# Optimization experiments

Hardware: AMD Instinct MI355X
Metric: run time of the kernel (lower is better)

The kernel has to match this reference:

```python
import jax, jax.numpy as jnp
import numpy as np

B, S, D, H = 2, 2048, 1024, 16
HD = D // H  # 64
ROPE_BASE = 10000.0


def _rope_tables(seq_len, head_dim):
    pos = jnp.arange(seq_len, dtype=jnp.float32)
    inv_freq = 1.0 / (ROPE_BASE ** (jnp.arange(0, head_dim, 2, dtype=jnp.float32) / head_dim))
    ang = pos[:, None] * inv_freq[None, :]            # [S, HD/2]
    emb = jnp.concatenate([ang, ang], axis=-1)        # [S, HD]
    return jnp.cos(emb), jnp.sin(emb)


def setup_inputs() -> dict:
    key = jax.random.key(0)
    k0, k1, k2 = jax.random.split(key, 3)
    x = jax.random.normal(k0, (B, S, D), dtype=jnp.float32)
    Wq = jax.random.normal(k1, (D, D), dtype=jnp.float32) * 0.02
    Wv = jax.random.normal(k2, (D, D), dtype=jnp.float32) * 0.02
    cos, sin = _rope_tables(S, HD)
    return {"x": x, "Wq": Wq, "Wv": Wv, "cos": cos, "sin": sin}


def _rotate_half(u):
    h = u.shape[-1] // 2
    return jnp.concatenate([-u[..., h:], u[..., :h]], axis=-1)


def reference(x, Wq, Wv, cos, sin):
    b, s, d = x.shape
    h, hd = H, d // H
    # NOTE: source module has xk = self.query(x) (key uses query weights) -- preserved.
    xq = (x @ Wq.T).reshape(b, s, h, hd)
    xk = (x @ Wq.T).reshape(b, s, h, hd)
    xv = (x @ Wv.T).reshape(b, s, h, hd)
    c = cos[None, :, None, :]  # [1,S,1,HD]
    sn = sin[None, :, None, :]
    q = xq * c + _rotate_half(xq) * sn
    k = xk * c + _rotate_half(xk) * sn
    q = q.transpose(0, 2, 1, 3)   # [B,H,S,HD]
    k = k.transpose(0, 2, 1, 3)
    v = xv.transpose(0, 2, 1, 3)
    scale = 1.0 / jnp.sqrt(jnp.asarray(hd, dtype=q.dtype))
    scores = jnp.einsum('bhqd,bhkd->bhqk', q, k) * scale  # [B,H,S,S]
    causal = jnp.tril(jnp.ones((s, s), dtype=bool))
    scores = jnp.where(causal[None, None, :, :], scores, jnp.finfo(scores.dtype).min)
    probs = jax.nn.softmax(scores, axis=-1)
    out = jnp.einsum('bhqk,bhkd->bhqd', probs, v)
    return out.transpose(0, 2, 1, 3).reshape(b, s, d)
```

## Files before the change

kernel.cpp:

```cpp
#include <hip/hip_runtime.h>


typedef float f32x4 __attribute__((ext_vector_type(4)));
typedef short s16x8 __attribute__((ext_vector_type(8)));

__device__ inline unsigned short f2bf(float f) {
  union { float f; unsigned u; } v; v.f = f;
  unsigned r = v.u + 0x7FFFu + ((v.u >> 16) & 1u);
  return (unsigned short)(r >> 16);
}

__device__ inline void gload16(const unsigned short* g, unsigned short* l) {
  __builtin_amdgcn_global_load_lds(
      (const __attribute__((address_space(1))) unsigned int*)g,
      (__attribute__((address_space(3))) unsigned int*)l, 16, 0, 0);
}

__global__ __launch_bounds__(256) void convert_all(
    const float* __restrict__ x, const float* __restrict__ wq,
    const float* __restrict__ wv, unsigned short* __restrict__ xb,
    unsigned short* __restrict__ wqb, unsigned short* __restrict__ wvb) {
  int i = blockIdx.x * 256 + threadIdx.x;
  const float* src; unsigned short* dst; int off;
  if (i < 1048576) { src = x; dst = xb; off = i; }
  else if (i < 1310720) { src = wq; dst = wqb; off = i - 1048576; }
  else { src = wv; dst = wvb; off = i - 1310720; }
  float4 v = ((const float4*)src)[off];
  ushort4 o;
  o.x = f2bf(v.x); o.y = f2bf(v.y); o.z = f2bf(v.z); o.w = f2bf(v.w);
  ((ushort4*)dst)[off] = o;
}

template <int IS_Q>
__global__ __launch_bounds__(256, 2) void qv_gemm(
    const unsigned short* __restrict__ A, const unsigned short* __restrict__ W,
    const float* __restrict__ cosT, const float* __restrict__ sinT,
    unsigned short* __restrict__ Out) {
  __shared__ unsigned short GS[2][2][128][64];
  int tid = threadIdx.x;
  int bm = blockIdx.x & 31, bn = blockIdx.x >> 5;
  int w = tid >> 6, lane = tid & 63, lr = lane & 15, lg = lane >> 4;
  int wm = w >> 1, wn = w & 1;
  int l8 = lane >> 3, l7 = lane & 7;
  f32x4 acc[4][4] = {};

  const unsigned short* srcbase =
      (w < 2) ? (A + bm * 128 * 1024) : (W + bn * 128 * 1024);
  int ab = w >> 1;

  auto stage = [&](int step) {
    int buf = step & 1, kt = step * 64;
#pragma unroll
    for (int i = 0; i < 8; ++i) {
      int rgrp = (w & 1) * 8 + i;
      int u = rgrp * 8 + l8;
      int ch = l7 ^ (u & 7);
      gload16(srcbase + u * 1024 + kt + ch * 8,
              (unsigned short*)&GS[buf][ab][rgrp * 8][0]);
    }
  };

  stage(0);
  for (int step = 0; step < 16; ++step) {
    int buf = step & 1;
    asm volatile("s_waitcnt vmcnt(0)" ::: "memory");
    __syncthreads();
    if (step + 1 < 16) stage(step + 1);
    s16x8 af[4][2], bfr[4][2];
#pragma unroll
    for (int mf = 0; mf < 4; ++mf)
#pragma unroll
      for (int kk = 0; kk < 2; ++kk)
        af[mf][kk] = *(const s16x8*)
            &GS[buf][0][wm * 64 + mf * 16 + lr][((kk * 4 + lg) ^ (lr & 7)) * 8];
#pragma unroll
    for (int nf = 0; nf < 4; ++nf)
#pragma unroll
      for (int kk = 0; kk < 2; ++kk)
        bfr[nf][kk] = *(const s16x8*)
            &GS[buf][1][wn * 64 + nf * 16 + lr][((kk * 4 + lg) ^ (lr & 7)) * 8];
#pragma unroll
    for (int mf = 0; mf < 4; ++mf)
#pragma unroll
      for (int nf = 0; nf < 4; ++nf)
#pragma unroll
        for (int kk = 0; kk < 2; ++kk)
          acc[mf][nf] = __builtin_amdgcn_mfma_f32_16x16x32_bf16(
              af[mf][kk], bfr[nf][kk], acc[mf][nf], 0, 0, 0);
  }

  int mBase = bm * 128 + wm * 64;
  int nBase = bn * 128 + wn * 64;
#pragma unroll
  for (int mf = 0; mf < 4; ++mf)
#pragma unroll
    for (int j = 0; j < 4; ++j) {
      int m = mBase + mf * 16 + 4 * lg + j;
      int b = m >> 11, s = m & 2047;
      if (IS_Q) {
#pragma unroll
        for (int nf = 0; nf < 4; ++nf) {
          int col = nBase + nf * 16 + lr;
          int h = col >> 6, hd = col & 63;
          float self = acc[mf][nf][j];
          float part = (nf < 2) ? -acc[mf][nf + 2][j] : acc[mf][nf - 2][j];
          float val = self * cosT[s * 64 + hd] + part * sinT[s * 64 + hd];
          Out[(((b * 16 + h) * 2048 + s) << 6) + hd] = f2bf(val);
        }
      } else {
#pragma unroll
        for (int nf = 0; nf < 4; ++nf) {
          int col = nBase + nf * 16 + lr;
          int h = col >> 6, hd = col & 63;
          Out[((b * 16 + h) * 64 + hd) * 2048 + s] = f2bf(acc[mf][nf][j]);
        }
      }
    }
}

__global__ __launch_bounds__(256, 2) void attn(
    const unsigned short* __restrict__ Qb,
    const unsigned short* __restrict__ Vt,
    float* __restrict__ out) {
  __shared__ unsigned short SM[2][2][2][64][64];
  const float SC = 0.125f * 1.44269504088896f;
  const float THR = 44.0f;
  int tid = threadIdx.x;
  int fid = blockIdx.x;
  int bh = 4 * (fid & 7) + ((fid >> 3) & 3);
  int qt = 31 - (fid >> 5);
  int w = tid >> 6, lane = tid & 63, lr = lane & 15, lg = lane >> 4;
  int l8 = lane >> 3, l7 = lane & 7;
  int q0 = qt * 64, qh = w >> 1, par = w & 1;
  const unsigned short* Qh = Qb + bh * (2048 * 64);
  const unsigned short* Vh = Vt + bh * (64 * 2048);

  s16x8 aq[2][2];
#pragma unroll
  for (int qs = 0; qs < 2; ++qs)
#pragma unroll
    for (int kk = 0; kk < 2; ++kk)
      aq[qs][kk] =
          *(const s16x8*)&Qh[(q0 + qh * 32 + 16 * qs + lr) * 64 + kk * 32 + lg * 8];

  f32x4 o[2][4] = {};
  float m_[2] = {-1e30f, -1e30f}, l_[2] = {0.f, 0.f};

  auto stage = [&](int ss) {
    int buf = ss & 1, k0 = ss * 128;
#pragma unroll
    for (int i = 0; i < 8; ++i) {
      int u = i * 8 + l8;
      int ch = l7 ^ (u & 7);
      const unsigned short* src;
      if (w < 2) {
        int g = (u & 0x23) | (((u >> 4) & 1) << 2) | (((u >> 3) & 1) << 4) |
                (((u >> 2) & 1) << 3);
        src = Qh + (k0 + par * 64 + g) * 64 + ch * 8;
      } else {
        src = Vh + u * 2048 + k0 + par * 64 + ch * 8;
      }
      gload16(src, (unsigned short*)&SM[buf][w >> 1][par][i * 8][0]);
    }
  };

  int nss = (qt >> 1) + 1;
  stage(0);
  for (int ss = 0; ss < nss; ++ss) {
    int buf = ss & 1;
    asm volatile("s_waitcnt vmcnt(0)" ::: "memory");
    __syncthreads();
    if (ss + 1 < nss) stage(ss + 1);
    int kt = 2 * ss + par;
    if (kt <= qt) {
      s16x8 kf[4][2];
#pragma unroll
      for (int nf = 0; nf < 4; ++nf)
#pragma unroll
        for (int kk = 0; kk < 2; ++kk)
          kf[nf][kk] = *(const s16x8*)
              &SM[buf][0][par][nf * 16 + lr][((kk * 4 + lg) ^ (lr & 7)) * 8];
      f32x4 sa[2][4];
#pragma unroll
      for (int qs = 0; qs < 2; ++qs)
#pragma unroll
        for (int nf = 0; nf < 4; ++nf) sa[qs][nf] = (f32x4){0.f, 0.f, 0.f, 0.f};
#pragma unroll
      for (int kk = 0; kk < 2; ++kk)
#pragma unroll
        for (int nf = 0; nf < 4; ++nf)
#pragma unroll
          for (int qs = 0; qs < 2; ++qs)
            sa[qs][nf] = __builtin_amdgcn_mfma_f32_16x16x32_bf16(
                kf[nf][kk], aq[qs][kk], sa[qs][nf], 0, 0, 0);
      if (kt == qt) {
#pragma unroll
        for (int qs = 0; qs < 2; ++qs) {
          int qglob = q0 + qh * 32 + 16 * qs + lr;
#pragma unroll
          for (int nf = 0; nf < 4; ++nf) {
            int kc = kt * 64 + 8 * lg + 4 * (nf & 1) + 32 * (nf >> 1);
#pragma unroll
            for (int j = 0; j < 4; ++j)
              if (kc + j > qglob) sa[qs][nf][j] = -3e38f;
          }
        }
      }
      float tm[2];
      float worst = -3e38f;
#pragma unroll
      for (int qs = 0; qs < 2; ++qs) {
        float t = sa[qs][0][0];
#pragma unroll
        for (int nf = 0; nf < 4; ++nf)
#pragma unroll
          for (int j = 0; j < 4; ++j) t = fmaxf(t, sa[qs][nf][j]);
        tm[qs] = t;
        worst = fmaxf(worst, t - m_[qs]);
      }
      if (!__all(worst <= THR)) {
#pragma unroll
        for (int qs = 0; qs < 2; ++qs) {
          float rm = fmaxf(tm[qs], __shfl_xor(tm[qs], 16));
          rm = fmaxf(rm, __shfl_xor(rm, 32));
          float mn = fmaxf(m_[qs], rm);
          float alpha = exp2f((m_[qs] - mn) * SC);
          m_[qs] = mn; l_[qs] *= alpha;
#pragma unroll
          for (int j = 0; j < 4; ++j) {
            float aj = __shfl(alpha, 4 * lg + j);
#pragma unroll
            for (int nf = 0; nf < 4; ++nf) o[qs][nf][j] *= aj;
          }
        }
      }
      unsigned cpk[2][8];
#pragma unroll
      for (int qs = 0; qs < 2; ++qs) {
        float msc = m_[qs] * SC;
#pragma unroll
        for (int nf = 0; nf < 4; ++nf) {
          float p0 = exp2f(fmaf(sa[qs][nf][0], SC, -msc));
          float p1 = exp2f(fmaf(sa[qs][nf][1], SC, -msc));
          float p2 = exp2f(fmaf(sa[qs][nf][2], SC, -msc));
          float p3 = exp2f(fmaf(sa[qs][nf][3], SC, -msc));
          l_[qs] += (p0 + p1) + (p2 + p3);
          unsigned r0, r1;
          asm("v_cvt_pk_bf16_f32 %0, %1, %2" : "=v"(r0) : "v"(p0), "v"(p1));
          asm("v_cvt_pk_bf16_f32 %0, %1, %2" : "=v"(r1) : "v"(p2), "v"(p3));
          cpk[qs][nf * 2] = r0; cpk[qs][nf * 2 + 1] = r1;
        }
      }
      s16x8 pav[2][2];
#pragma unroll
      for (int qs = 0; qs < 2; ++qs)
#pragma unroll
        for (int kk = 0; kk < 2; ++kk) {
          union { unsigned u[4]; s16x8 v; } pa;
          pa.u[0] = cpk[qs][4 * kk + 0]; pa.u[1] = cpk[qs][4 * kk + 1];
          pa.u[2] = cpk[qs][4 * kk + 2]; pa.u[3] = cpk[qs][4 * kk + 3];
          pav[qs][kk] = pa.v;
        }
#pragma unroll
      for (int kk = 0; kk < 2; ++kk)
#pragma unroll
        for (int nf = 0; nf < 4; ++nf) {
          s16x8 vf = *(const s16x8*)
              &SM[buf][1][par][nf * 16 + lr][((kk * 4 + lg) ^ (lr & 7)) * 8];
#pragma unroll
          for (int qs = 0; qs < 2; ++qs)
            o[qs][nf] = __builtin_amdgcn_mfma_f32_16x16x32_bf16(
                pav[qs][kk], vf, o[qs][nf], 0, 0, 0);
        }
    }
  }

  __syncthreads();
  float* MB = (float*)SM;
  float* ML = MB + 4352;
  int pair = qh;
#pragma unroll
  for (int qs = 0; qs < 2; ++qs) {
    float t = l_[qs];
    t += __shfl_xor(t, 16); t += __shfl_xor(t, 32);
    l_[qs] = t;
  }
  if (par) {
#pragma unroll
    for (int qs = 0; qs < 2; ++qs) {
#pragma unroll
      for (int nf = 0; nf < 4; ++nf)
#pragma unroll
        for (int j = 0; j < 4; ++j)
          MB[(((pair * 2 + qs) * 4 + nf) * 16 + 4 * lg + j) * 17 + lr] = o[qs][nf][j];
      if (lg == 0) {
        ML[((pair * 2 + qs) * 2 + 0) * 16 + lr] = m_[qs];
        ML[((pair * 2 + qs) * 2 + 1) * 16 + lr] = l_[qs];
      }
    }
  }
  __syncthreads();
  if (!par) {
    int b = bh >> 4, h = bh & 15;
#pragma unroll
    for (int qs = 0; qs < 2; ++qs) {
      float m1 = ML[((pair * 2 + qs) * 2 + 0) * 16 + lr];
      float l1 = ML[((pair * 2 + qs) * 2 + 1) * 16 + lr];
      float ms = fmaxf(m_[qs], m1);
      float a0 = exp2f((m_[qs] - ms) * SC), a1 = exp2f((m1 - ms) * SC);
      float inv = 1.0f / (a0 * l_[qs] + a1 * l1);
#pragma unroll
      for (int j = 0; j < 4; ++j) {
        float c0 = __shfl(a0 * inv, 4 * lg + j);
        float c1 = __shfl(a1 * inv, 4 * lg + j);
#pragma unroll
        for (int nf = 0; nf < 4; ++nf) {
          float o1 = MB[(((pair * 2 + qs) * 4 + nf) * 16 + 4 * lg + j) * 17 + lr];
          int q = q0 + pair * 32 + 16 * qs + 4 * lg + j;
          out[(b * 2048 + q) * 1024 + h * 64 + nf * 16 + lr] =
              c0 * o[qs][nf][j] + c1 * o1;
        }
      }
    }
  }
}

extern "C" void kernel_launch(void* const* d_in, const int* in_sizes, int n_in,
                              void* d_out, int out_size, void* d_ws, size_t ws_size,
                              hipStream_t stream) {
  const float* x = (const float*)d_in[0];
  const float* Wq = (const float*)d_in[1];
  const float* Wv = (const float*)d_in[2];
  const float* cosT = (const float*)d_in[3];
  const float* sinT = (const float*)d_in[4];
  float* out = (float*)d_out;

  unsigned short* xb = (unsigned short*)d_ws;
  unsigned short* wqb = xb + 4 * 1024 * 1024;
  unsigned short* wvb = wqb + 1024 * 1024;
  unsigned short* Qb = wvb + 1024 * 1024;
  unsigned short* Vtb = Qb + 4 * 1024 * 1024;

  convert_all<<<6144, 256, 0, stream>>>(x, Wq, Wv, xb, wqb, wvb);

  qv_gemm<1><<<256, 256, 0, stream>>>(xb, wqb, cosT, sinT, Qb);
  qv_gemm<0><<<256, 256, 0, stream>>>(xb, wvb, cosT, sinT, Vtb);

  attn<<<1024, 256, 0, stream>>>(Qb, Vtb, out);
}
```

Baseline: 79.60 us.

## Store K/V in MFMA fragment layout and load attention operands directly to registers

```diff
diff --git a/kernel.cpp b/kernel.cpp
--- a/kernel.cpp
+++ b/kernel.cpp
@@ -31,21 +31,24 @@
   ((ushort4*)dst)[off] = o;
 }
 
-template <int IS_Q>
 __global__ __launch_bounds__(256, 2) void qv_gemm(
-    const unsigned short* __restrict__ A, const unsigned short* __restrict__ W,
-    const float* __restrict__ cosT, const float* __restrict__ sinT,
-    unsigned short* __restrict__ Out) {
+    const unsigned short* __restrict__ A, const unsigned short* __restrict__ Wq,
+    const unsigned short* __restrict__ Wv, const float* __restrict__ cosT,
+    const float* __restrict__ sinT, unsigned short* __restrict__ Kf,
+    unsigned short* __restrict__ Vf) {
   __shared__ unsigned short GS[2][2][128][64];
   int tid = threadIdx.x;
-  int bm = blockIdx.x & 31, bn = blockIdx.x >> 5;
+  int isq = blockIdx.x < 256;
+  int b256 = blockIdx.x & 255;
+  int bm = b256 & 31, bn = b256 >> 5;
   int w = tid >> 6, lane = tid & 63, lr = lane & 15, lg = lane >> 4;
   int wm = w >> 1, wn = w & 1;
   int l8 = lane >> 3, l7 = lane & 7;
   f32x4 acc[4][4] = {};
 
+  const unsigned short* Wp = isq ? Wq : Wv;
   const unsigned short* srcbase =
-      (w < 2) ? (A + bm * 128 * 1024) : (W + bn * 128 * 1024);
+      (w < 2) ? (A + bm * 128 * 1024) : (Wp + bn * 128 * 1024);
   int ab = w >> 1;
 
   auto stage = [&](int step) {
@@ -91,13 +94,17 @@
 
   int mBase = bm * 128 + wm * 64;
   int nBase = bn * 128 + wn * 64;
-#pragma unroll
-  for (int mf = 0; mf < 4; ++mf)
-#pragma unroll
-    for (int j = 0; j < 4; ++j) {
-      int m = mBase + mf * 16 + 4 * lg + j;
-      int b = m >> 11, s = m & 2047;
-      if (IS_Q) {
+  if (isq) {
+#pragma unroll
+    for (int mf = 0; mf < 4; ++mf)
+#pragma unroll
+      for (int j = 0; j < 4; ++j) {
+        int m = mBase + mf * 16 + 4 * lg + j;
+        int b = m >> 11, s = m & 2047;
+        int w64 = s & 63, kt = s >> 6;
+        int nfk = ((w64 >> 5) << 1) | ((w64 >> 2) & 1);
+        int r31 = w64 & 31;
+        int lr2 = ((r31 >> 3) << 2) | (r31 & 3);
 #pragma unroll
         for (int nf = 0; nf < 4; ++nf) {
           int col = nBase + nf * 16 + lr;
@@ -105,24 +112,42 @@
           float self = acc[mf][nf][j];
           float part = (nf < 2) ? -acc[mf][nf + 2][j] : acc[mf][nf - 2][j];
           float val = self * cosT[s * 64 + hd] + part * sinT[s * 64 + hd];
-          Out[(((b * 16 + h) * 2048 + s) << 6) + hd] = f2bf(val);
+          int bh = b * 16 + h;
+          int kk = hd >> 5, lg2 = (hd >> 3) & 3, e = hd & 7;
+          int idx = (((((bh * 32 + kt) * 4 + nfk) * 2 + kk) * 64) +
+                     lg2 * 16 + lr2) * 8 + e;
+          Kf[idx] = f2bf(val);
         }
-      } else {
-#pragma unroll
-        for (int nf = 0; nf < 4; ++nf) {
-          int col = nBase + nf * 16 + lr;
-          int h = col >> 6, hd = col & 63;
-          Out[((b * 16 + h) * 64 + hd) * 2048 + s] = f2bf(acc[mf][nf][j]);
-        }
-      }
-    }
+      }
+  } else {
+#pragma unroll
+    for (int mf = 0; mf < 4; ++mf) {
+      int m0 = mBase + mf * 16 + 4 * lg;
+      int b = m0 >> 11, s0 = m0 & 2047;
+      int kt = s0 >> 6, w0 = s0 & 63;
+      int kkv = w0 >> 5, lg2 = (w0 >> 3) & 3, e0 = w0 & 7;
+#pragma unroll
+      for (int nf = 0; nf < 4; ++nf) {
+        int col = nBase + nf * 16 + lr;
+        int h = col >> 6;
+        int bh = b * 16 + h;
+        ushort4 pk;
+        pk.x = f2bf(acc[mf][nf][0]); pk.y = f2bf(acc[mf][nf][1]);
+        pk.z = f2bf(acc[mf][nf][2]); pk.w = f2bf(acc[mf][nf][3]);
+        int idx = (((((bh * 32 + kt) * 4 + nf) * 2 + kkv) * 64) +
+                   lg2 * 16 + lr) * 8 + e0;
+        *(ushort4*)&Vf[idx] = pk;
+      }
+    }
+  }
 }
 
 __global__ __launch_bounds__(256, 2) void attn(
-    const unsigned short* __restrict__ Qb,
-    const unsigned short* __restrict__ Vt,
+    const unsigned short* __restrict__ Kf,
+    const unsigned short* __restrict__ Vf,
     float* __restrict__ out) {
-  __shared__ unsigned short SM[2][2][2][64][64];
+  __shared__ float MB[2][2][4][16][17];
+  __shared__ float ML[2][2][2][16];
   const float SC = 0.125f * 1.44269504088896f;
   const float THR = 44.0f;
   int tid = threadIdx.x;
@@ -130,155 +155,148 @@
   int bh = 4 * (fid & 7) + ((fid >> 3) & 3);
   int qt = 31 - (fid >> 5);
   int w = tid >> 6, lane = tid & 63, lr = lane & 15, lg = lane >> 4;
-  int l8 = lane >> 3, l7 = lane & 7;
   int q0 = qt * 64, qh = w >> 1, par = w & 1;
-  const unsigned short* Qh = Qb + bh * (2048 * 64);
-  const unsigned short* Vh = Vt + bh * (64 * 2048);
+
+  const unsigned short* KfB = Kf + (size_t)bh * 32 * 4096;
+  const unsigned short* VfB = Vf + (size_t)bh * 32 * 4096;
 
   s16x8 aq[2][2];
 #pragma unroll
-  for (int qs = 0; qs < 2; ++qs)
+  for (int qs = 0; qs < 2; ++qs) {
+    int qr = q0 + qh * 32 + 16 * qs + lr;
+    int ktq = qr >> 6, w64 = qr & 63;
+    int nfq = ((w64 >> 5) << 1) | ((w64 >> 2) & 1);
+    int r31 = w64 & 31;
+    int lr2 = ((r31 >> 3) << 2) | (r31 & 3);
 #pragma unroll
     for (int kk = 0; kk < 2; ++kk)
-      aq[qs][kk] =
-          *(const s16x8*)&Qh[(q0 + qh * 32 + 16 * qs + lr) * 64 + kk * 32 + lg * 8];
+      aq[qs][kk] = *(const s16x8*)
+          &KfB[((((ktq * 4 + nfq) * 2 + kk) * 64) + lg * 16 + lr2) * 8];
+  }
 
   f32x4 o[2][4] = {};
   float m_[2] = {-1e30f, -1e30f}, l_[2] = {0.f, 0.f};
 
-  auto stage = [&](int ss) {
-    int buf = ss & 1, k0 = ss * 128;
-#pragma unroll
-    for (int i = 0; i < 8; ++i) {
-      int u = i * 8 + l8;
-      int ch = l7 ^ (u & 7);
-      const unsigned short* src;
-      if (w < 2) {
-        int g = (u & 0x23) | (((u >> 4) & 1) << 2) | (((u >> 3) & 1) << 4) |
-                (((u >> 2) & 1) << 3);
-        src = Qh + (k0 + par * 64 + g) * 64 + ch * 8;
-      } else {
-        src = Vh + u * 2048 + k0 + par * 64 + ch * 8;
-      }
-      gload16(src, (unsigned short*)&SM[buf][w >> 1][par][i * 8][0]);
-    }
+  s16x8 kf[4][2], vf[4][2];
+  auto loadK = [&](int kt) {
+#pragma unroll
+    for (int nf = 0; nf < 4; ++nf)
+#pragma unroll
+      for (int kk = 0; kk < 2; ++kk)
+        kf[nf][kk] = *(const s16x8*)
+            &KfB[(((kt * 4 + nf) * 2 + kk) * 64 + lane) * 8];
   };
-
-  int nss = (qt >> 1) + 1;
-  stage(0);
-  for (int ss = 0; ss < nss; ++ss) {
-    int buf = ss & 1;
-    asm volatile("s_waitcnt vmcnt(0)" ::: "memory");
-    __syncthreads();
-    if (ss + 1 < nss) stage(ss + 1);
-    int kt = 2 * ss + par;
-    if (kt <= qt) {
-      s16x8 kf[4][2];
-#pragma unroll
-      for (int nf = 0; nf < 4; ++nf)
-#pragma unroll
-        for (int kk = 0; kk < 2; ++kk)
-          kf[nf][kk] = *(const s16x8*)
-              &SM[buf][0][par][nf * 16 + lr][((kk * 4 + lg) ^ (lr & 7)) * 8];
-      f32x4 sa[2][4];
-#pragma unroll
-      for (int qs = 0; qs < 2; ++qs)
-#pragma unroll
-        for (int nf = 0; nf < 4; ++nf) sa[qs][nf] = (f32x4){0.f, 0.f, 0.f, 0.f};
+  auto loadV = [&](int kt) {
+#pragma unroll
+    for (int nf = 0; nf < 4; ++nf)
 #pragma unroll
       for (int kk = 0; kk < 2; ++kk)
-#pragma unroll
-        for (int nf = 0; nf < 4; ++nf)
-#pragma unroll
-          for (int qs = 0; qs < 2; ++qs)
-            sa[qs][nf] = __builtin_amdgcn_mfma_f32_16x16x32_bf16(
-                kf[nf][kk], aq[qs][kk], sa[qs][nf], 0, 0, 0);
-      if (kt == qt) {
-#pragma unroll
-        for (int qs = 0; qs < 2; ++qs) {
-          int qglob = q0 + qh * 32 + 16 * qs + lr;
-#pragma unroll
-          for (int nf = 0; nf < 4; ++nf) {
-            int kc = kt * 64 + 8 * lg + 4 * (nf & 1) + 32 * (nf >> 1);
-#pragma unroll
-            for (int j = 0; j < 4; ++j)
-              if (kc + j > qglob) sa[qs][nf][j] = -3e38f;
-          }
+        vf[nf][kk] = *(const s16x8*)
+            &VfB[(((kt * 4 + nf) * 2 + kk) * 64 + lane) * 8];
+  };
+
+  int kt = par;
+  bool active = kt <= qt;
+  if (active) { loadK(kt); loadV(kt); }
+  while (active) {
+    f32x4 sa[2][4];
+#pragma unroll
+    for (int qs = 0; qs < 2; ++qs)
+#pragma unroll
+      for (int nf = 0; nf < 4; ++nf) sa[qs][nf] = (f32x4){0.f, 0.f, 0.f, 0.f};
+#pragma unroll
+    for (int kk = 0; kk < 2; ++kk)
+#pragma unroll
+      for (int nf = 0; nf < 4; ++nf)
+#pragma unroll
+        for (int qs = 0; qs < 2; ++qs)
+          sa[qs][nf] = __builtin_amdgcn_mfma_f32_16x16x32_bf16(
+              kf[nf][kk], aq[qs][kk], sa[qs][nf], 0, 0, 0);
+
+    int ktn = kt + 2;
+    bool more = ktn <= qt;
+    if (more) loadK(ktn);
+
+    if (kt == qt) {
+#pragma unroll
+      for (int qs = 0; qs < 2; ++qs) {
+        int qglob = q0 + qh * 32 + 16 * qs + lr;
+#pragma unroll
+        for (int nf = 0; nf < 4; ++nf) {
+          int kc = kt * 64 + 8 * lg + 4 * (nf & 1) + 32 * (nf >> 1);
+#pragma unroll
+          for (int j = 0; j < 4; ++j)
+            if (kc + j > qglob) sa[qs][nf][j] = -3e38f;
         }
       }
-      float tm[2];
-      float worst = -3e38f;
+    }
+    float tm[2];
+    float worst = -3e38f;
+#pragma unroll
+    for (int qs = 0; qs < 2; ++qs) {
+      float t = sa[qs][0][0];
+#pragma unroll
+      for (int nf = 0; nf < 4; ++nf)
+#pragma unroll
+        for (int j = 0; j < 4; ++j) t = fmaxf(t, sa[qs][nf][j]);
+      tm[qs] = t;
+      worst = fmaxf(worst, t - m_[qs]);
+    }
+    if (!__all(worst <= THR)) {
 #pragma unroll
       for (int qs = 0; qs < 2; ++qs) {
-        float t = sa[qs][0][0];
-#pragma unroll
-        for (int nf = 0; nf < 4; ++nf)
-#pragma unroll
-          for (int j = 0; j < 4; ++j) t = fmaxf(t, sa[qs][nf][j]);
-        tm[qs] = t;
-        worst = fmaxf(worst, t - m_[qs]);
-      }
-      if (!__all(worst <= THR)) {
-#pragma unroll
-        for (int qs = 0; qs < 2; ++qs) {
-          float rm = fmaxf(tm[qs], __shfl_xor(tm[qs], 16));
-          rm = fmaxf(rm, __shfl_xor(rm, 32));
-          float mn = fmaxf(m_[qs], rm);
-          float alpha = exp2f((m_[qs] - mn) * SC);
-          m_[qs] = mn; l_[qs] *= alpha;
-#pragma unroll
-          for (int j = 0; j < 4; ++j) {
-            float aj = __shfl(alpha, 4 * lg + j);
-#pragma unroll
-            for (int nf = 0; nf < 4; ++nf) o[qs][nf][j] *= aj;
-          }
+        float rm = fmaxf(tm[qs], __shfl_xor(tm[qs], 16));
+        rm = fmaxf(rm, __shfl_xor(rm, 32));
+        float mn = fmaxf(m_[qs], rm);
+        float alpha = exp2f((m_[qs] - mn) * SC);
+        m_[qs] = mn; l_[qs] *= alpha;
+#pragma unroll
+        for (int j = 0; j < 4; ++j) {
+          float aj = __shfl(alpha, 4 * lg + j);
+#pragma unroll
+          for (int nf = 0; nf < 4; ++nf) o[qs][nf][j] *= aj;
         }
       }
-      unsigned cpk[2][8];
-#pragma unroll
-      for (int qs = 0; qs < 2; ++qs) {
-        float msc = m_[qs] * SC;
-#pragma unroll
-        for (int nf = 0; nf < 4; ++nf) {
-          float p0 = exp2f(fmaf(sa[qs][nf][0], SC, -msc));
-          float p1 = exp2f(fmaf(sa[qs][nf][1], SC, -msc));
-          float p2 = exp2f(fmaf(sa[qs][nf][2], SC, -msc));
-          float p3 = exp2f(fmaf(sa[qs][nf][3], SC, -msc));
-          l_[qs] += (p0 + p1) + (p2 + p3);
-          unsigned r0, r1;
-          asm("v_cvt_pk_bf16_f32 %0, %1, %2" : "=v"(r0) : "v"(p0), "v"(p1));
-          asm("v_cvt_pk_bf16_f32 %0, %1, %2" : "=v"(r1) : "v"(p2), "v"(p3));
-          cpk[qs][nf * 2] = r0; cpk[qs][nf * 2 + 1] = r1;
-        }
-      }
-      s16x8 pav[2][2];
-#pragma unroll
-      for (int qs = 0; qs < 2; ++qs)
-#pragma unroll
-        for (int kk = 0; kk < 2; ++kk) {
-          union { unsigned u[4]; s16x8 v; } pa;
-          pa.u[0] = cpk[qs][4 * kk + 0]; pa.u[1] = cpk[qs][4 * kk + 1];
-          pa.u[2] = cpk[qs][4 * kk + 2]; pa.u[3] = cpk[qs][4 * kk + 3];
-          pav[qs][kk] = pa.v;
-        }
-#pragma unroll
-      for (int kk = 0; kk < 2; ++kk)
-#pragma unroll
-        for (int nf = 0; nf < 4; ++nf) {
-          s16x8 vf = *(const s16x8*)
-              &SM[buf][1][par][nf * 16 + lr][((kk * 4 + lg) ^ (lr & 7)) * 8];
-#pragma unroll
-          for (int qs = 0; qs < 2; ++qs)
-            o[qs][nf] = __builtin_amdgcn_mfma_f32_16x16x32_bf16(
-                pav[qs][kk], vf, o[qs][nf], 0, 0, 0);
-        }
-    }
-  }
-
-  __syncthreads();
-  float* MB = (float*)SM;
-  float* ML = MB + 4352;
-  int pair = qh;
+    }
+    unsigned cpk[2][8];
+#pragma unroll
+    for (int qs = 0; qs < 2; ++qs) {
+      float msc = m_[qs] * SC;
+#pragma unroll
+      for (int nf = 0; nf < 4; ++nf) {
+        float p0 = exp2f(fmaf(sa[qs][nf][0], SC, -msc));
+        float p1 = exp2f(fmaf(sa[qs][nf][1], SC, -msc));
+        float p2 = exp2f(fmaf(sa[qs][nf][2], SC, -msc));
+        float p3 = exp2f(fmaf(sa[qs][nf][3], SC, -msc));
+        l_[qs] += (p0 + p1) + (p2 + p3);
+        unsigned r0, r1;
+        asm("v_cvt_pk_bf16_f32 %0, %1, %2" : "=v"(r0) : "v"(p0), "v"(p1));
+        asm("v_cvt_pk_bf16_f32 %0, %1, %2" : "=v"(r1) : "v"(p2), "v"(p3));
+        cpk[qs][nf * 2] = r0; cpk[qs][nf * 2 + 1] = r1;
+      }
+    }
+    s16x8 pav[2][2];
+#pragma unroll
+    for (int qs = 0; qs < 2; ++qs)
+#pragma unroll
+      for (int kk = 0; kk < 2; ++kk) {
+        union { unsigned u[4]; s16x8 v; } pa;
+        pa.u[0] = cpk[qs][4 * kk + 0]; pa.u[1] = cpk[qs][4 * kk + 1];
+        pa.u[2] = cpk[qs][4 * kk + 2]; pa.u[3] = cpk[qs][4 * kk + 3];
+        pav[qs][kk] = pa.v;
+      }
+#pragma unroll
+    for (int kk = 0; kk < 2; ++kk)
+#pragma unroll
+      for (int nf = 0; nf < 4; ++nf)
+#pragma unroll
+        for (int qs = 0; qs < 2; ++qs)
+          o[qs][nf] = __builtin_amdgcn_mfma_f32_16x16x32_bf16(
+              pav[qs][kk], vf[nf][kk], o[qs][nf], 0, 0, 0);
+    if (more) loadV(ktn);
+    kt = ktn; active = more;
+  }
+
 #pragma unroll
   for (int qs = 0; qs < 2; ++qs) {
     float t = l_[qs];
@@ -292,10 +310,10 @@
       for (int nf = 0; nf < 4; ++nf)
 #pragma unroll
         for (int j = 0; j < 4; ++j)
-          MB[(((pair * 2 + qs) * 4 + nf) * 16 + 4 * lg + j) * 17 + lr] = o[qs][nf][j];
+          MB[qh][qs][nf][4 * lg + j][lr] = o[qs][nf][j];
       if (lg == 0) {
-        ML[((pair * 2 + qs) * 2 + 0) * 16 + lr] = m_[qs];
-        ML[((pair * 2 + qs) * 2 + 1) * 16 + lr] = l_[qs];
+        ML[qh][qs][0][lr] = m_[qs];
+        ML[qh][qs][1][lr] = l_[qs];
       }
     }
   }
@@ -304,8 +322,8 @@
     int b = bh >> 4, h = bh & 15;
 #pragma unroll
     for (int qs = 0; qs < 2; ++qs) {
-      float m1 = ML[((pair * 2 + qs) * 2 + 0) * 16 + lr];
-      float l1 = ML[((pair * 2 + qs) * 2 + 1) * 16 + lr];
+      float m1 = ML[qh][qs][0][lr];
+      float l1 = ML[qh][qs][1][lr];
       float ms = fmaxf(m_[qs], m1);
       float a0 = exp2f((m_[qs] - ms) * SC), a1 = exp2f((m1 - ms) * SC);
       float inv = 1.0f / (a0 * l_[qs] + a1 * l1);
@@ -315,8 +333,8 @@
         float c1 = __shfl(a1 * inv, 4 * lg + j);
 #pragma unroll
         for (int nf = 0; nf < 4; ++nf) {
-          float o1 = MB[(((pair * 2 + qs) * 4 + nf) * 16 + 4 * lg + j) * 17 + lr];
-          int q = q0 + pair * 32 + 16 * qs + 4 * lg + j;
+          float o1 = MB[qh][qs][nf][4 * lg + j][lr];
+          int q = q0 + qh * 32 + 16 * qs + 4 * lg + j;
           out[(b * 2048 + q) * 1024 + h * 64 + nf * 16 + lr] =
               c0 * o[qs][nf][j] + c1 * o1;
         }
@@ -338,13 +356,10 @@
   unsigned short* xb = (unsigned short*)d_ws;
   unsigned short* wqb = xb + 4 * 1024 * 1024;
   unsigned short* wvb = wqb + 1024 * 1024;
-  unsigned short* Qb = wvb + 1024 * 1024;
-  unsigned short* Vtb = Qb + 4 * 1024 * 1024;
+  unsigned short* Kfb = wvb + 1024 * 1024;
+  unsigned short* Vfb = Kfb + 4 * 1024 * 1024;
 
   convert_all<<<6144, 256, 0, stream>>>(x, Wq, Wv, xb, wqb, wvb);
-
-  qv_gemm<1><<<256, 256, 0, stream>>>(xb, wqb, cosT, sinT, Qb);
-  qv_gemm<0><<<256, 256, 0, stream>>>(xb, wvb, cosT, sinT, Vtb);
-
-  attn<<<1024, 256, 0, stream>>>(Qb, Vtb, out);
-}
+  qv_gemm<<<512, 256, 0, stream>>>(xb, wqb, wvb, cosT, sinT, Kfb, Vfb);
+  attn<<<1024, 256, 0, stream>>>(Kfb, Vfb, out);
+}
```

New measurement: 66.29 us. -16.7%, faster.
